# Kernel tuning notes

Hardware: AMD Instinct MI355X
Metric: run time of the kernel (lower is better)

Reference implementation:

```python
import jax, jax.numpy as jnp
import numpy as np


def exp_mix_frac(p1, p2, a1, b1, a2, b2):
    # stable merge of two (numerator, denominator) pairs carried in log-scale p
    p = jnp.maximum(p1, p2)
    e1 = jnp.exp(p1 - p)
    e2 = jnp.exp(p2 - p)
    return a1 * e1 + a2 * e2, b1 * e1 + b2 * e2, p


def assoc_reduce_step(left, right):
    akv_l, ak_l, w_l, p_l = left
    akv_r, ak_r, w_r, p_r = right
    a, b, p = exp_mix_frac(p_l + w_r, p_r, akv_l, ak_l, akv_r, ak_r)
    return a, b, w_l + w_r, p


def setup_inputs() -> dict:
    key = jax.random.key(0)
    ks = jax.random.split(key, 7)
    S, B, E = 2048, 8, 1024
    scale = 1.0 / np.sqrt(E)
    return {
        "x": jax.random.normal(ks[0], (S, B, E), jnp.float32),
        "tmrkv": jax.random.uniform(ks[1], (3 * E,), jnp.float32),
        "Wk": jax.random.normal(ks[2], (E, E), jnp.float32) * scale,
        "Wv": jax.random.normal(ks[3], (E, E), jnp.float32) * scale,
        "time_decay": jax.random.normal(ks[4], (E,), jnp.float32) - 1.0,
        "time_first": jax.random.normal(ks[5], (E,), jnp.float32),
        "Wout": jax.random.normal(ks[6], (E, E), jnp.float32) * scale,
    }


def reference(x, tmrkv, Wk, Wv, time_decay, time_first, Wout):
    # x: (S, B, E) time-major (batch_first=False path of the source module)
    S, B, E = x.shape
    x_prev = jnp.concatenate([jnp.zeros_like(x[:1]), x[:-1]], axis=0)
    # time_mix_rkv layout: [r | k | v]; r-branch is computed in the source but
    # never used in the associative-scan path, so it is omitted (same output).
    mk = tmrkv[E:2 * E]
    mv = tmrkv[2 * E:]
    k = (mk * x + (1.0 - mk) * x_prev) @ Wk  # (S, B, E)
    v = (mv * x + (1.0 - mv) * x_prev) @ Wv  # (S, B, E)

    k_ = k.reshape(S, B * E)
    v_ = v.reshape(S, B * E)
    W_ = jnp.broadcast_to(jnp.tile(time_decay, B)[None, :], (S, B * E))
    ones = jnp.ones_like(v_)
    # log-depth parallel scan over time with numerically-stable exp merge
    a_, b_, _, p_ = jax.lax.associative_scan(
        assoc_reduce_step, (v_, ones, W_, k_), axis=0)

    a_state = a_.reshape(S, B, E)
    b_state = b_.reshape(S, B, E)
    p_state = p_.reshape(S, B, E)
    c, d, _ = exp_mix_frac(p_state, k + time_first + time_decay,
                           a_state, b_state, v, jnp.ones_like(v))
    rwkv = c / d  # (S, B, E)
    return rwkv @ Wout
```

## Files before the change

kernel.cpp:

```cpp
#include <hip/hip_runtime.h>
#include <stdint.h>

#define S_LEN  2048
#define B_DIM  8
#define E_DIM  1024
#define BE     (B_DIM * E_DIM)
#define M_ROWS (S_LEN * B_DIM)
#define NCHUNK 64
#define CLEN   (S_LEN / NCHUNK)

typedef __attribute__((ext_vector_type(8))) short bf16x8;
typedef __attribute__((ext_vector_type(4))) float f32x4;
typedef __attribute__((ext_vector_type(16))) float f32x16;

__device__ __forceinline__ unsigned short f2bf(float f) {
    unsigned int u = __float_as_uint(f);
    u += 0x7FFFu + ((u >> 16) & 1u);
    return (unsigned short)(u >> 16);
}
__device__ __forceinline__ float bf_lo(unsigned int u) {
    return __uint_as_float(u << 16);
}
__device__ __forceinline__ float bf_hi(unsigned int u) {
    return __uint_as_float(u & 0xFFFF0000u);
}

__global__ __launch_bounds__(256) void mix_kernel(
    const float* __restrict__ x, const float* __restrict__ tmrkv,
    unsigned short* __restrict__ xk, unsigned short* __restrict__ xv)
{
    int i = blockIdx.x * 256 + threadIdx.x;
    const float4* x4 = (const float4*)x;
    float4 xc[2], xp[2];
    xc[0] = x4[2 * i];
    xc[1] = x4[2 * i + 1];
    if (i >= BE / 8) {
        xp[0] = x4[2 * i - BE / 4];
        xp[1] = x4[2 * i + 1 - BE / 4];
    } else {
        xp[0] = make_float4(0.f, 0.f, 0.f, 0.f);
        xp[1] = make_float4(0.f, 0.f, 0.f, 0.f);
    }
    int e4 = (2 * i) & (E_DIM / 4 - 1);
    ushort4 ok[2], ov[2];
    #pragma unroll
    for (int h = 0; h < 2; ++h) {
        float4 mk = ((const float4*)(tmrkv + E_DIM))[e4 + h];
        float4 mv = ((const float4*)(tmrkv + 2 * E_DIM))[e4 + h];
        ok[h].x = f2bf(mk.x * xc[h].x + (1.f - mk.x) * xp[h].x);
        ok[h].y = f2bf(mk.y * xc[h].y + (1.f - mk.y) * xp[h].y);
        ok[h].z = f2bf(mk.z * xc[h].z + (1.f - mk.z) * xp[h].z);
        ok[h].w = f2bf(mk.w * xc[h].w + (1.f - mk.w) * xp[h].w);
        ov[h].x = f2bf(mv.x * xc[h].x + (1.f - mv.x) * xp[h].x);
        ov[h].y = f2bf(mv.y * xc[h].y + (1.f - mv.y) * xp[h].y);
        ov[h].z = f2bf(mv.z * xc[h].z + (1.f - mv.z) * xp[h].z);
        ov[h].w = f2bf(mv.w * xc[h].w + (1.f - mv.w) * xp[h].w);
    }
    ((ushort4*)xk)[2 * i]     = ok[0];
    ((ushort4*)xk)[2 * i + 1] = ok[1];
    ((ushort4*)xv)[2 * i]     = ov[0];
    ((ushort4*)xv)[2 * i + 1] = ov[1];
}

__global__ __launch_bounds__(256) void cast_transpose_k(
    const float* __restrict__ w0, const float* __restrict__ w1,
    const float* __restrict__ w2,
    unsigned short* __restrict__ o0, unsigned short* __restrict__ o1,
    unsigned short* __restrict__ o2)
{
    const float* in = blockIdx.z == 0 ? w0 : (blockIdx.z == 1 ? w1 : w2);
    unsigned short* out = blockIdx.z == 0 ? o0 : (blockIdx.z == 1 ? o1 : o2);
    __shared__ float tile[32][33];
    int bx = blockIdx.x * 32, by = blockIdx.y * 32;
    int tx = threadIdx.x, ty = threadIdx.y;
    #pragma unroll
    for (int i = 0; i < 32; i += 8)
        tile[ty + i][tx] = in[(size_t)(by + ty + i) * E_DIM + bx + tx];
    __syncthreads();
    #pragma unroll
    for (int i = 0; i < 32; i += 8)
        out[(size_t)(bx + ty + i) * E_DIM + by + tx] = f2bf(tile[tx][ty + i]);
}

#define BM 256
#define BN 256
#define BK 64

__device__ __forceinline__ void stage_plane(unsigned short* lds_base, int buf_plane,
                                            const unsigned short* gsrc, int K, int wave)
{
    #pragma unroll
    for (int s = 0; s < 2; ++s) {
        const unsigned short* g = gsrc + (size_t)s * 128 * K;
        unsigned short* l = lds_base + buf_plane * 8192 + s * 4096 + wave * 512;
        __builtin_amdgcn_global_load_lds(
            (const __attribute__((address_space(1))) unsigned int*)g,
            (__attribute__((address_space(3))) unsigned int*)l, 16, 0, 0);
    }
}

__device__ __forceinline__ void swz_xy(int& bx, int& by)
{
    int hw   = blockIdx.x + gridDim.x * blockIdx.y;
    int xcd  = hw & 7;
    int slot = hw >> 3;
    bx = xcd * 8 + (slot & 7);
    by = slot >> 3;
}

template <typename OutT>
__device__ __forceinline__ void gemm_body(
    const unsigned short* __restrict__ A,
    const unsigned short* __restrict__ BT,
    OutT* __restrict__ C, int M, int N, int K, int bxt, int byt)
{
    __shared__ __align__(16) unsigned short smem[2][4][8192];
    const int tid  = threadIdx.x;
    const int wave = tid >> 6, lane = tid & 63;
    const int l31 = lane & 31, lh = lane >> 5;
    const int wm = wave >> 2, wn = wave & 3;
    const int bm = bxt * BM, bn = byt * BN;

    const int srow = tid >> 2;
    const int sg   = (tid & 3) ^ ((srow >> 1) & 3);
    const unsigned short* sAp = A  + (size_t)(bm + srow) * K + sg * 8;
    const unsigned short* sBp = BT + (size_t)(bn + srow) * K + sg * 8;
    unsigned short* lb = &smem[0][0][0];

    f32x16 acc[4][2];
    #pragma unroll
    for (int i = 0; i < 4; ++i)
        #pragma unroll
        for (int j = 0; j < 2; ++j)
            #pragma unroll
            for (int e = 0; e < 16; ++e)
                acc[i][j][e] = 0.f;

    bf16x8 af[2][2], bfr[2][2];

#define GATE_(n)                                                              \
    asm volatile("s_waitcnt lgkmcnt(0)" ::: "memory");                        \
    asm volatile("s_waitcnt vmcnt(" #n ")" ::: "memory");                     \
    __builtin_amdgcn_s_barrier();                                             \
    asm volatile("" ::: "memory");

#define LDA2_(h, mh)                                                          \
    _Pragma("unroll")                                                         \
    for (int ii = 0; ii < 2; ++ii)                                            \
        _Pragma("unroll")                                                     \
        for (int s = 0; s < 2; ++s) {                                         \
            int R = wm * 128 + (2 * (mh) + ii) * 32 + l31;                    \
            int g = s * 2 + lh;                                               \
            af[ii][s] = *(const bf16x8*)&smem[cur][(h) * 2]                   \
                [R * 32 + ((g ^ ((R >> 1) & 3)) << 3)];                       \
        }
#define LDB2_(h)                                                              \
    _Pragma("unroll")                                                         \
    for (int jj = 0; jj < 2; ++jj)                                            \
        _Pragma("unroll")                                                     \
        for (int s = 0; s < 2; ++s) {                                         \
            int R = wn * 64 + jj * 32 + l31;                                  \
            int g = s * 2 + lh;                                               \
            bfr[jj][s] = *(const bf16x8*)&smem[cur][(h) * 2 + 1]              \
                [R * 32 + ((g ^ ((R >> 1) & 3)) << 3)];                       \
        }
#define MMA2_(mh)                                                             \
    __builtin_amdgcn_s_setprio(1);                                            \
    _Pragma("unroll")                                                         \
    for (int ii = 0; ii < 2; ++ii)                                            \
        _Pragma("unroll")                                                     \
        for (int jj = 0; jj < 2; ++jj)                                        \
            _Pragma("unroll")                                                 \
            for (int s = 0; s < 2; ++s)                                       \
                acc[2 * (mh) + ii][jj] =                                      \
                    __builtin_amdgcn_mfma_f32_32x32x16_bf16(                  \
                        af[ii][s], bfr[jj][s], acc[2 * (mh) + ii][jj],        \
                        0, 0, 0);                                             \
    __builtin_amdgcn_s_setprio(0);

    const int nk = K / BK;
    stage_plane(lb, 0, sAp,      K, wave);
    stage_plane(lb, 1, sBp,      K, wave);
    stage_plane(lb, 2, sAp + 32, K, wave);
    stage_plane(lb, 3, sBp + 32, K, wave);

    int cur = 0;
    for (int t = 0; t < nk - 1; ++t) {
        const int nxt = cur ^ 1;
        const unsigned short* nA = sAp + (size_t)(t + 1) * BK;
        const unsigned short* nB = sBp + (size_t)(t + 1) * BK;
        GATE_(4);
        LDA2_(0, 0); LDB2_(0);
        stage_plane(lb, nxt * 4 + 0, nA, K, wave);
        MMA2_(0);
        LDA2_(0, 1);
        stage_plane(lb, nxt * 4 + 1, nB, K, wave);
        MMA2_(1);
        GATE_(4);
        LDA2_(1, 0); LDB2_(1);
        stage_plane(lb, nxt * 4 + 2, nA + 32, K, wave);
        MMA2_(0);
        LDA2_(1, 1);
        stage_plane(lb, nxt * 4 + 3, nB + 32, K, wave);
        MMA2_(1);
        cur = nxt;
    }
    GATE_(4);
    LDA2_(0, 0); LDB2_(0);
    MMA2_(0);
    LDA2_(0, 1);
    MMA2_(1);
    GATE_(0);
    LDA2_(1, 0); LDB2_(1);
    MMA2_(0);
    LDA2_(1, 1);
    MMA2_(1);

    #pragma unroll
    for (int i = 0; i < 4; ++i)
        #pragma unroll
        for (int j = 0; j < 2; ++j)
            #pragma unroll
            for (int r = 0; r < 16; ++r) {
                int row = bm + wm * 128 + i * 32 + (r & 3) + 8 * (r >> 2) + 4 * lh;
                int col = bn + wn * 64 + j * 32 + l31;
                if constexpr (sizeof(OutT) == 2)
                    C[(size_t)row * N + col] = f2bf(acc[i][j][r]);
                else
                    C[(size_t)row * N + col] = acc[i][j][r];
            }
#undef GATE_
#undef LDA2_
#undef LDB2_
#undef MMA2_
}

__global__ __launch_bounds__(512, 2) void gemm_kv(
    const unsigned short* __restrict__ A0, const unsigned short* __restrict__ B0,
    unsigned short* __restrict__ C0,
    const unsigned short* __restrict__ A1, const unsigned short* __restrict__ B1,
    unsigned short* __restrict__ C1, int M, int N, int K)
{
    int bx, by;
    swz_xy(bx, by);
    if (blockIdx.z == 0) gemm_body<unsigned short>(A0, B0, C0, M, N, K, bx, by);
    else                 gemm_body<unsigned short>(A1, B1, C1, M, N, K, bx, by);
}

__global__ __launch_bounds__(512, 2) void gemm_out(
    const unsigned short* __restrict__ A, const unsigned short* __restrict__ BT,
    float* __restrict__ C, int M, int N, int K)
{
    int bx, by;
    swz_xy(bx, by);
    gemm_body<float>(A, BT, C, M, N, K, bx, by);
}

__device__ __forceinline__ void wkv_step(float& a, float& b, float& p,
                                         float kt, float vt, float w)
{
    float pw = p + w;
    float pn = fmaxf(pw, kt);
    float e1 = __expf(pw - pn), e2 = __expf(kt - pn);
    a = a * e1 + vt * e2;
    b = b * e1 + e2;
    p = pn;
}

#define Q_PER_T (BE / 4)

__global__ __launch_bounds__(256) void scan_pass1(
    const uint2* __restrict__ k4, const uint2* __restrict__ v4,
    const float* __restrict__ tdec,
    float4* __restrict__ sA, float4* __restrict__ sB, float4* __restrict__ sP)
{
    int g = blockIdx.x * 256 + threadIdx.x;
    int q = g & (Q_PER_T - 1);
    int c = g >> 11;
    float4 w4 = ((const float4*)tdec)[q & (E_DIM / 4 - 1)];
    size_t idx = (size_t)c * CLEN * Q_PER_T + q;
    uint2 ku = k4[idx], vu = v4[idx];
    float a0 = bf_lo(vu.x), b0 = 1.f, p0 = bf_lo(ku.x);
    float a1 = bf_hi(vu.x), b1 = 1.f, p1 = bf_hi(ku.x);
    float a2 = bf_lo(vu.y), b2 = 1.f, p2 = bf_lo(ku.y);
    float a3 = bf_hi(vu.y), b3 = 1.f, p3 = bf_hi(ku.y);
    for (int j = 1; j < CLEN; ++j) {
        idx += Q_PER_T;
        ku = k4[idx]; vu = v4[idx];
        wkv_step(a0, b0, p0, bf_lo(ku.x), bf_lo(vu.x), w4.x);
        wkv_step(a1, b1, p1, bf_hi(ku.x), bf_hi(vu.x), w4.y);
        wkv_step(a2, b2, p2, bf_lo(ku.y), bf_lo(vu.y), w4.z);
        wkv_step(a3, b3, p3, bf_hi(ku.y), bf_hi(vu.y), w4.w);
    }
    sA[g] = make_float4(a0, a1, a2, a3);
    sB[g] = make_float4(b0, b1, b2, b3);
    sP[g] = make_float4(p0, p1, p2, p3);
}

__global__ __launch_bounds__(256) void scan_pass2(
    const float* __restrict__ tdec,
    float* __restrict__ sA, float* __restrict__ sB, float* __restrict__ sP)
{
    __shared__ float tA[64 * 65], tB[64 * 65], tP[64 * 65];
    const int t   = threadIdx.x;
    const int ch0 = blockIdx.x * 64;
    const int chl = t & 63;
    const int cq  = t >> 6;
    #pragma unroll 4
    for (int cc = 0; cc < 16; ++cc) {
        int c = cq * 16 + cc;
        int idx = c * BE + ch0 + chl;
        tA[chl * 65 + c] = sA[idx];
        tB[chl * 65 + c] = sB[idx];
        tP[chl * 65 + c] = sP[idx];
    }
    __syncthreads();
    const int lane = t & 63, wave = t >> 6;
    for (int i = 0; i < 16; ++i) {
        int ch = wave * 16 + i;
        float w = tdec[(ch0 + ch) & (E_DIM - 1)];
        float a = tA[ch * 65 + lane];
        float b = tB[ch * 65 + lane];
        float p = tP[ch * 65 + lane];
        float W = (float)CLEN * w;
        #pragma unroll
        for (int d = 1; d < 64; d <<= 1) {
            float a_l = __shfl_up(a, d);
            float b_l = __shfl_up(b, d);
            float p_l = __shfl_up(p, d);
            float W_l = __shfl_up(W, d);
            if (lane >= d) {
                float pw = p_l + W;
                float pn = fmaxf(pw, p);
                float e1 = __expf(pw - pn), e2 = __expf(p - pn);
                a = a_l * e1 + a * e2;
                b = b_l * e1 + b * e2;
                p = pn;
                W = W_l + W;
            }
        }
        float ea = __shfl_up(a, 1);
        float eb = __shfl_up(b, 1);
        float ep = __shfl_up(p, 1);
        if (lane == 0) { ea = 0.f; eb = 0.f; ep = -__builtin_inff(); }
        tA[ch * 65 + lane] = ea;
        tB[ch * 65 + lane] = eb;
        tP[ch * 65 + lane] = ep;
    }
    __syncthreads();
    #pragma unroll 4
    for (int cc = 0; cc < 16; ++cc) {
        int c = cq * 16 + cc;
        int idx = c * BE + ch0 + chl;
        sA[idx] = tA[chl * 65 + c];
        sB[idx] = tB[chl * 65 + c];
        sP[idx] = tP[chl * 65 + c];
    }
}

__global__ __launch_bounds__(256) void scan_pass3(
    const uint2* __restrict__ k4, const uint2* __restrict__ v4,
    const float* __restrict__ tdec, const float* __restrict__ tfir,
    const float4* __restrict__ sA, const float4* __restrict__ sB,
    const float4* __restrict__ sP, uint2* __restrict__ rwkv4)
{
    int g = blockIdx.x * 256 + threadIdx.x;
    int q = g & (Q_PER_T - 1);
    int c = g >> 11;
    int e4 = q & (E_DIM / 4 - 1);
    float4 w4 = ((const float4*)tdec)[e4];
    float4 f4 = ((const float4*)tfir)[e4];
    float u0 = f4.x + w4.x, u1 = f4.y + w4.y;
    float u2 = f4.z + w4.z, u3 = f4.w + w4.w;
    float4 av = sA[g], bv = sB[g], pv = sP[g];
    float a0 = av.x, b0 = bv.x, p0 = pv.x;
    float a1 = av.y, b1 = bv.y, p1 = pv.y;
    float a2 = av.z, b2 = bv.z, p2 = pv.z;
    float a3 = av.w, b3 = bv.w, p3 = pv.w;
    size_t idx = (size_t)c * CLEN * Q_PER_T + q;
    for (int j = 0; j < CLEN; ++j) {
        uint2 ku = k4[idx], vu = v4[idx];
        float kt0 = bf_lo(ku.x), vt0 = bf_lo(vu.x);
        float kt1 = bf_hi(ku.x), vt1 = bf_hi(vu.x);
        float kt2 = bf_lo(ku.y), vt2 = bf_lo(vu.y);
        float kt3 = bf_hi(ku.y), vt3 = bf_hi(vu.y);
        wkv_step(a0, b0, p0, kt0, vt0, w4.x);
        wkv_step(a1, b1, p1, kt1, vt1, w4.y);
        wkv_step(a2, b2, p2, kt2, vt2, w4.z);
        wkv_step(a3, b3, p3, kt3, vt3, w4.w);
        float kb0 = kt0 + u0, kb1 = kt1 + u1, kb2 = kt2 + u2, kb3 = kt3 + u3;
        float q0 = fmaxf(p0, kb0), q1 = fmaxf(p1, kb1);
        float q2 = fmaxf(p2, kb2), q3 = fmaxf(p3, kb3);
        float g0 = __expf(p0 - q0), h0 = __expf(kb0 - q0);
        float g1 = __expf(p1 - q1), h1 = __expf(kb1 - q1);
        float g2 = __expf(p2 - q2), h2 = __expf(kb2 - q2);
        float g3 = __expf(p3 - q3), h3 = __expf(kb3 - q3);
        float r0 = (a0 * g0 + vt0 * h0) / (b0 * g0 + h0);
        float r1 = (a1 * g1 + vt1 * h1) / (b1 * g1 + h1);
        float r2 = (a2 * g2 + vt2 * h2) / (b2 * g2 + h2);
        float r3 = (a3 * g3 + vt3 * h3) / (b3 * g3 + h3);
        uint2 o;
        o.x = (unsigned int)f2bf(r0) | ((unsigned int)f2bf(r1) << 16);
        o.y = (unsigned int)f2bf(r2) | ((unsigned int)f2bf(r3) << 16);
        rwkv4[idx] = o;
        idx += Q_PER_T;
    }
}

extern "C" void kernel_launch(void* const* d_in, const int* in_sizes, int n_in,
                              void* d_out, int out_size, void* d_ws, size_t ws_size,
                              hipStream_t stream)
{
    const float* x     = (const float*)d_in[0];
    const float* tmrkv = (const float*)d_in[1];
    const float* Wk    = (const float*)d_in[2];
    const float* Wv    = (const float*)d_in[3];
    const float* tdec  = (const float*)d_in[4];
    const float* tfir  = (const float*)d_in[5];
    const float* Wout  = (const float*)d_in[6];
    float* out = (float*)d_out;

    char* ws = (char*)d_ws;
    const size_t SZ_BF = (size_t)M_ROWS * E_DIM * 2;
    unsigned short* xk   = (unsigned short*)(ws);
    unsigned short* xv   = (unsigned short*)(ws + SZ_BF);
    unsigned short* kbuf = (unsigned short*)(ws + 2 * SZ_BF);
    unsigned short* vbuf = (unsigned short*)(ws + 3 * SZ_BF);
    unsigned short* WkT  = (unsigned short*)(ws + 4 * SZ_BF);
    unsigned short* WvT  = WkT + (size_t)E_DIM * E_DIM;
    unsigned short* WoutT= WvT + (size_t)E_DIM * E_DIM;
    float* sA = (float*)xv;
    float* sB = sA + (size_t)NCHUNK * BE;
    float* sP = sB + (size_t)NCHUNK * BE;
    unsigned short* rwkv = xk;

    mix_kernel<<<(M_ROWS * E_DIM / 8) / 256, 256, 0, stream>>>(x, tmrkv, xk, xv);

    dim3 tb(32, 8), tg(E_DIM / 32, E_DIM / 32, 3);
    cast_transpose_k<<<tg, tb, 0, stream>>>(Wk, Wv, Wout, WkT, WvT, WoutT);

    dim3 gkv(M_ROWS / BM, E_DIM / BN, 2);
    gemm_kv<<<gkv, 512, 0, stream>>>(xk, WkT, kbuf, xv, WvT, vbuf,
                                     M_ROWS, E_DIM, E_DIM);

    scan_pass1<<<(NCHUNK * Q_PER_T) / 256, 256, 0, stream>>>(
        (const uint2*)kbuf, (const uint2*)vbuf, tdec,
        (float4*)sA, (float4*)sB, (float4*)sP);
    scan_pass2<<<BE / 64, 256, 0, stream>>>(tdec, sA, sB, sP);
    scan_pass3<<<(NCHUNK * Q_PER_T) / 256, 256, 0, stream>>>(
        (const uint2*)kbuf, (const uint2*)vbuf, tdec, tfir,
        (const float4*)sA, (const float4*)sB, (const float4*)sP,
        (uint2*)rwkv);

    dim3 gg(M_ROWS / BM, E_DIM / BN);
    gemm_out<<<gg, 512, 0, stream>>>(rwkv, WoutT, out, M_ROWS, E_DIM, E_DIM);
}
```

Measured before the change: 315.1 us.

## Restructure GEMM LDS staging to full-K-tile planes with one prefetch per iteration

Result: faster. 307.4 us (-2.5%).

```diff
diff --git a/kernel.cpp b/kernel.cpp
--- a/kernel.cpp
+++ b/kernel.cpp
@@ -86,13 +86,14 @@
 #define BN 256
 #define BK 64
 
-__device__ __forceinline__ void stage_plane(unsigned short* lds_base, int buf_plane,
-                                            const unsigned short* gsrc, int K, int wave)
-{
-    #pragma unroll
-    for (int s = 0; s < 2; ++s) {
-        const unsigned short* g = gsrc + (size_t)s * 128 * K;
-        unsigned short* l = lds_base + buf_plane * 8192 + s * 4096 + wave * 512;
+__device__ __forceinline__ void stage_tile(unsigned short* lds_plane,
+                                           const unsigned short* gsrc,
+                                           int K, int wave)
+{
+    #pragma unroll
+    for (int s = 0; s < 4; ++s) {
+        const unsigned short* g = gsrc + (size_t)s * 64 * K;
+        unsigned short* l = lds_plane + s * 4096 + wave * 512;
         __builtin_amdgcn_global_load_lds(
             (const __attribute__((address_space(1))) unsigned int*)g,
             (__attribute__((address_space(3))) unsigned int*)l, 16, 0, 0);
@@ -114,18 +115,17 @@
     const unsigned short* __restrict__ BT,
     OutT* __restrict__ C, int M, int N, int K, int bxt, int byt)
 {
-    __shared__ __align__(16) unsigned short smem[2][4][8192];
+    __shared__ __align__(16) unsigned short smem[2][2][16384];
     const int tid  = threadIdx.x;
     const int wave = tid >> 6, lane = tid & 63;
     const int l31 = lane & 31, lh = lane >> 5;
     const int wm = wave >> 2, wn = wave & 3;
     const int bm = bxt * BM, bn = byt * BN;
 
-    const int srow = tid >> 2;
-    const int sg   = (tid & 3) ^ ((srow >> 1) & 3);
+    const int srow = tid >> 3;
+    const int sg   = (tid & 7) ^ (srow & 7);
     const unsigned short* sAp = A  + (size_t)(bm + srow) * K + sg * 8;
     const unsigned short* sBp = BT + (size_t)(bn + srow) * K + sg * 8;
-    unsigned short* lb = &smem[0][0][0];
 
     f32x16 acc[4][2];
     #pragma unroll
@@ -138,21 +138,15 @@
 
     bf16x8 af[2][2], bfr[2][2];
 
-#define GATE_(n)                                                              \
-    asm volatile("s_waitcnt lgkmcnt(0)" ::: "memory");                        \
-    asm volatile("s_waitcnt vmcnt(" #n ")" ::: "memory");                     \
-    __builtin_amdgcn_s_barrier();                                             \
-    asm volatile("" ::: "memory");
-
 #define LDA2_(h, mh)                                                          \
     _Pragma("unroll")                                                         \
     for (int ii = 0; ii < 2; ++ii)                                            \
         _Pragma("unroll")                                                     \
         for (int s = 0; s < 2; ++s) {                                         \
             int R = wm * 128 + (2 * (mh) + ii) * 32 + l31;                    \
-            int g = s * 2 + lh;                                               \
-            af[ii][s] = *(const bf16x8*)&smem[cur][(h) * 2]                   \
-                [R * 32 + ((g ^ ((R >> 1) & 3)) << 3)];                       \
+            int c = (h) * 4 + s * 2 + lh;                                     \
+            af[ii][s] = *(const bf16x8*)&smem[cur][0]                         \
+                [R * 64 + ((c ^ (R & 7)) << 3)];                              \
         }
 #define LDB2_(h)                                                              \
     _Pragma("unroll")                                                         \
@@ -160,9 +154,9 @@
         _Pragma("unroll")                                                     \
         for (int s = 0; s < 2; ++s) {                                         \
             int R = wn * 64 + jj * 32 + l31;                                  \
-            int g = s * 2 + lh;                                               \
-            bfr[jj][s] = *(const bf16x8*)&smem[cur][(h) * 2 + 1]              \
-                [R * 32 + ((g ^ ((R >> 1) & 3)) << 3)];                       \
+            int c = (h) * 4 + s * 2 + lh;                                     \
+            bfr[jj][s] = *(const bf16x8*)&smem[cur][1]                        \
+                [R * 64 + ((c ^ (R & 7)) << 3)];                              \
         }
 #define MMA2_(mh)                                                             \
     __builtin_amdgcn_s_setprio(1);                                            \
@@ -177,44 +171,36 @@
                         af[ii][s], bfr[jj][s], acc[2 * (mh) + ii][jj],        \
                         0, 0, 0);                                             \
     __builtin_amdgcn_s_setprio(0);
+#define COMPUTE_()                                                            \
+    LDB2_(0); LDA2_(0, 0); MMA2_(0);                                          \
+    LDA2_(0, 1);           MMA2_(1);                                          \
+    LDB2_(1); LDA2_(1, 0); MMA2_(0);                                          \
+    LDA2_(1, 1);           MMA2_(1);
 
     const int nk = K / BK;
-    stage_plane(lb, 0, sAp,      K, wave);
-    stage_plane(lb, 1, sBp,      K, wave);
-    stage_plane(lb, 2, sAp + 32, K, wave);
-    stage_plane(lb, 3, sBp + 32, K, wave);
+    stage_tile(&smem[0][0][0], sAp, K, wave);
+    stage_tile(&smem[0][1][0], sBp, K, wave);
 
     int cur = 0;
     for (int t = 0; t < nk - 1; ++t) {
         const int nxt = cur ^ 1;
-        const unsigned short* nA = sAp + (size_t)(t + 1) * BK;
-        const unsigned short* nB = sBp + (size_t)(t + 1) * BK;
-        GATE_(4);
-        LDA2_(0, 0); LDB2_(0);
-        stage_plane(lb, nxt * 4 + 0, nA, K, wave);
-        MMA2_(0);
-        LDA2_(0, 1);
-        stage_plane(lb, nxt * 4 + 1, nB, K, wave);
-        MMA2_(1);
-        GATE_(4);
-        LDA2_(1, 0); LDB2_(1);
-        stage_plane(lb, nxt * 4 + 2, nA + 32, K, wave);
-        MMA2_(0);
-        LDA2_(1, 1);
-        stage_plane(lb, nxt * 4 + 3, nB + 32, K, wave);
-        MMA2_(1);
+        asm volatile("s_waitcnt lgkmcnt(0)" ::: "memory");
+        __builtin_amdgcn_s_barrier();
+        asm volatile("" ::: "memory");
+        stage_tile(&smem[nxt][0][0], sAp + (size_t)(t + 1) * BK, K, wave);
+        stage_tile(&smem[nxt][1][0], sBp + (size_t)(t + 1) * BK, K, wave);
+        asm volatile("s_waitcnt vmcnt(8)" ::: "memory");
+        __builtin_amdgcn_s_barrier();
+        asm volatile("" ::: "memory");
+        COMPUTE_();
         cur = nxt;
     }
-    GATE_(4);
-    LDA2_(0, 0); LDB2_(0);
-    MMA2_(0);
-    LDA2_(0, 1);
-    MMA2_(1);
-    GATE_(0);
-    LDA2_(1, 0); LDB2_(1);
-    MMA2_(0);
-    LDA2_(1, 1);
-    MMA2_(1);
+    asm volatile("s_waitcnt lgkmcnt(0)" ::: "memory");
+    __builtin_amdgcn_s_barrier();
+    asm volatile("s_waitcnt vmcnt(0)" ::: "memory");
+    __builtin_amdgcn_s_barrier();
+    asm volatile("" ::: "memory");
+    COMPUTE_();
 
     #pragma unroll
     for (int i = 0; i < 4; ++i)
@@ -229,10 +215,10 @@
                 else
                     C[(size_t)row * N + col] = acc[i][j][r];
             }
-#undef GATE_
 #undef LDA2_
 #undef LDB2_
 #undef MMA2_
+#undef COMPUTE_
 }
 
 __global__ __launch_bounds__(512, 2) void gemm_kv(
```
